# Kernel optimization log

Measured on AMD Instinct MI355X. Metric: run time of the kernel, lower is better.

The kernel has to match this reference:

```python
import jax, jax.numpy as jnp
import numpy as np
from jax import lax

SEQ_LEN, PRED_LEN, D_MODEL, ENC_IN, D_FF, N_LAYERS, N_HEADS = 336, 192, 512, 64, 2048, 2, 8
NUM_STEPS, COF, MARK, B, LABEL_LEN = 2, 0.1, 4, 32, 48


def _pos_emb(T, D):
    pos = np.arange(T)[:, None].astype(np.float32)
    div = np.exp(np.arange(0, D, 2).astype(np.float32) * (-np.log(10000.0) / D))
    pe = np.zeros((T, D), np.float32)
    pe[:, 0::2] = np.sin(pos * div)
    pe[:, 1::2] = np.cos(pos * div)
    return jnp.asarray(pe)


def _layer_norm(x, g, b):
    mu = x.mean(-1, keepdims=True)
    var = ((x - mu) ** 2).mean(-1, keepdims=True)
    return (x - mu) * lax.rsqrt(var + 1e-5) * g + b


def _embed(x, mark, conv_w, tf_w):
    # TokenEmbedding: circular Conv1d(kernel=3, pad=1) over time, no bias
    T = x.shape[1]
    xp = jnp.concatenate([x[:, -1:], x, x[:, :1]], axis=1)  # circular pad
    tok = sum(jnp.einsum('btc,cd->btd', xp[:, k:k + T], conv_w[k]) for k in range(3))
    return tok + _pos_emb(T, conv_w.shape[2])[None] + mark @ tf_w


def _block(x, p):
    Wq, Wk, Wv, Wo, bq, bk, bv, bo, g1, be1, W1, b1, W2, b2, g2, be2 = p
    Bb, T, D = x.shape
    dh = D // N_HEADS
    q = (x @ Wq + bq).reshape(Bb, T, N_HEADS, dh)
    k = (x @ Wk + bk).reshape(Bb, T, N_HEADS, dh)
    v = (x @ Wv + bv).reshape(Bb, T, N_HEADS, dh)
    att = jax.nn.softmax(jnp.einsum('bthd,bshd->bhts', q, k) / jnp.sqrt(jnp.float32(dh)), axis=-1)
    o = jnp.einsum('bhts,bshd->bthd', att, v).reshape(Bb, T, D) @ Wo + bo
    x = _layer_norm(x + o, g1, be1)
    ff = jax.nn.relu(x @ W1 + b1) @ W2 + b2
    return _layer_norm(x + ff, g2, be2)


def _gru(x, h, wih, whh, bih, bhh):
    gi = x @ wih.T + bih
    gh = h @ whh.T + bhh
    ir, iz, inn = jnp.split(gi, 3, axis=-1)
    hr, hz, hn = jnp.split(gh, 3, axis=-1)
    r = jax.nn.sigmoid(ir + hr)
    z = jax.nn.sigmoid(iz + hz)
    n = jnp.tanh(inn + r * hn)
    return (1.0 - z) * n + z * h


def _langevin(corrupt, cond, hx0, gru_p, score_w, alpha):
    # per-step GRU + energy-gradient update (Langevin refinement)
    def step(hx, xc):
        xi, ci = xc  # [B,C] each
        def energy(ri):
            h = _gru(jnp.concatenate([ri, ci], -1), hx, *gru_p)
            return (h @ score_w).sum() * COF, h
        g, h_new = jax.grad(energy, has_aux=True)(xi)
        return h_new, xi - alpha * g
    _, out = lax.scan(step, hx0, (corrupt.transpose(1, 0, 2), cond.transpose(1, 0, 2)))
    return out.transpose(1, 0, 2)  # [B,P,C]


def _forward(x_enc, x_mark_enc, batch_y, batch_y_mark, hx_init, token_conv_w, timefeat_w,
             Wq, Wk, Wv, Wo, bq, bk, bv, bo, ln1_g, ln1_b, W1, b1, W2, b2, ln2_g, ln2_b,
             pl1_w, pl1_b, pl2_w, pl2_b, proj_w, proj_b,
             gru_wih, gru_whh, gru_bih, gru_bhh, score_w, alpha):
    means = lax.stop_gradient(x_enc.mean(1, keepdims=True))
    xe = x_enc - means
    stdev = jnp.sqrt(xe.var(1, keepdims=True) + 1e-5)  # not detached in torch code
    xe = xe / stdev
    # predict_linear1 over time axis: [B,T,C] -> [B,P,C]
    pre = jnp.einsum('btc,pt->bpc', xe, pl1_w) + pl1_b[None, :, None]
    ymark = batch_y_mark[:, -PRED_LEN:, :]
    gru_p = (gru_wih, gru_whh, gru_bih, gru_bhh)
    local_loss = jnp.float32(0.0)
    out_dn = None
    for s in range(NUM_STEPS):
        corrupt = lax.stop_gradient(pre)
        corrupt = jnp.einsum('bpc,qp->bqc', corrupt, pl2_w) + pl2_b[None, :, None]
        emb = _embed(corrupt, ymark, token_conv_w, timefeat_w)
        for l in range(N_LAYERS):
            emb = _block(emb, (Wq[l], Wk[l], Wv[l], Wo[l], bq[l], bk[l], bv[l], bo[l],
                               ln1_g[l], ln1_b[l], W1[l], b1[l], W2[l], b2[l], ln2_g[l], ln2_b[l]))
        cond = emb @ proj_w.T + proj_b
        out = _langevin(corrupt, cond, hx_init[s], gru_p, score_w, alpha)
        pre = out
        out_dn = out * stdev[:, 0, :][:, None, :] + means[:, 0, :][:, None, :]
        local_loss = local_loss + jnp.mean(jnp.abs(out_dn - batch_y[:, -PRED_LEN:, :]))
    return out_dn, local_loss


def setup_inputs() -> dict:
    key = jax.random.key(0)
    ks = iter(jax.random.split(key, 64))
    r = lambda shape, s=0.02: jax.random.normal(next(ks), shape, dtype=jnp.float32) * s
    inp = dict(
        x_enc=jax.random.normal(next(ks), (B, SEQ_LEN, ENC_IN), dtype=jnp.float32),
        x_mark_enc=jax.random.normal(next(ks), (B, SEQ_LEN, MARK), dtype=jnp.float32),
        batch_y=jax.random.normal(next(ks), (B, LABEL_LEN + PRED_LEN, ENC_IN), dtype=jnp.float32),
        batch_y_mark=jax.random.normal(next(ks), (B, LABEL_LEN + PRED_LEN, MARK), dtype=jnp.float32),
        hx_init=jax.random.normal(next(ks), (NUM_STEPS, B, D_MODEL), dtype=jnp.float32),
        token_conv_w=r((3, ENC_IN, D_MODEL)),
        timefeat_w=r((MARK, D_MODEL)),
        Wq=r((N_LAYERS, D_MODEL, D_MODEL)), Wk=r((N_LAYERS, D_MODEL, D_MODEL)),
        Wv=r((N_LAYERS, D_MODEL, D_MODEL)), Wo=r((N_LAYERS, D_MODEL, D_MODEL)),
        bq=jnp.zeros((N_LAYERS, D_MODEL)), bk=jnp.zeros((N_LAYERS, D_MODEL)),
        bv=jnp.zeros((N_LAYERS, D_MODEL)), bo=jnp.zeros((N_LAYERS, D_MODEL)),
        ln1_g=jnp.ones((N_LAYERS, D_MODEL)), ln1_b=jnp.zeros((N_LAYERS, D_MODEL)),
        W1=r((N_LAYERS, D_MODEL, D_FF)), b1=jnp.zeros((N_LAYERS, D_FF)),
        W2=r((N_LAYERS, D_FF, D_MODEL)), b2=jnp.zeros((N_LAYERS, D_MODEL)),
        ln2_g=jnp.ones((N_LAYERS, D_MODEL)), ln2_b=jnp.zeros((N_LAYERS, D_MODEL)),
        pl1_w=r((PRED_LEN, SEQ_LEN), 0.05), pl1_b=jnp.zeros((PRED_LEN,)),
        pl2_w=r((PRED_LEN, PRED_LEN), 0.05), pl2_b=jnp.zeros((PRED_LEN,)),
        proj_w=r((ENC_IN, D_MODEL)), proj_b=jnp.zeros((ENC_IN,)),
        gru_wih=r((3 * D_MODEL, 2 * ENC_IN), 0.04), gru_whh=r((3 * D_MODEL, D_MODEL), 0.04),
        gru_bih=jnp.zeros((3 * D_MODEL,)), gru_bhh=jnp.zeros((3 * D_MODEL,)),
        score_w=r((D_MODEL,), 0.04),
        alpha=jnp.array([0.1], dtype=jnp.float32),
    )
    return inp


def reference(x_enc, x_mark_enc, batch_y, batch_y_mark, hx_init, token_conv_w, timefeat_w,
              Wq, Wk, Wv, Wo, bq, bk, bv, bo, ln1_g, ln1_b, W1, b1, W2, b2, ln2_g, ln2_b,
              pl1_w, pl1_b, pl2_w, pl2_b, proj_w, proj_b,
              gru_wih, gru_whh, gru_bih, gru_bhh, score_w, alpha):
    out, loss = _forward(x_enc, x_mark_enc, batch_y, batch_y_mark, hx_init, token_conv_w, timefeat_w,
                         Wq, Wk, Wv, Wo, bq, bk, bv, bo, ln1_g, ln1_b, W1, b1, W2, b2, ln2_g, ln2_b,
                         pl1_w, pl1_b, pl2_w, pl2_b, proj_w, proj_b,
                         gru_wih, gru_whh, gru_bih, gru_bhh, score_w, alpha)
    return out[:, -PRED_LEN:, :], loss
```

## Files before the change

kernel.cpp:

```cpp
#include <hip/hip_runtime.h>
#include <math.h>

#define BATCH 32
#define TT    192
#define DM    512
#define CIN   64
#define SEQL  336
#define DFF   2048
#define NH    8
#define COF   0.1f
#define OUTN  (BATCH*TT*CIN)

typedef _Float16 h2_t __attribute__((ext_vector_type(2)));
union H2U { unsigned int u; h2_t h; };

typedef short bf16x8 __attribute__((ext_vector_type(8)));
typedef float f32x4 __attribute__((ext_vector_type(4)));
typedef unsigned int u32x4 __attribute__((ext_vector_type(4)));

__device__ __forceinline__ unsigned short f2bf(float v) {
  union { float f; unsigned int u; } a; a.f = v;
  unsigned int r = (a.u + 0x7fffu + ((a.u >> 16) & 1u)) >> 16;
  return (unsigned short)r;
}

__device__ __forceinline__ int sd4(unsigned int a, unsigned int b, int c) {
#if __has_builtin(__builtin_amdgcn_sdot4)
  return __builtin_amdgcn_sdot4((int)a, (int)b, c, false);
#else
  c += (int)(signed char)(a & 0xff) * (int)(signed char)(b & 0xff);
  c += (int)(signed char)((a >> 8) & 0xff) * (int)(signed char)((b >> 8) & 0xff);
  c += (int)(signed char)((a >> 16) & 0xff) * (int)(signed char)((b >> 16) & 0xff);
  c += (int)(signed char)(a >> 24) * (int)(signed char)(b >> 24);
  return c;
#endif
}

__device__ __forceinline__ int sd16(u32x4 w, u32x4 h, int acc) {
  acc = sd4(w[0], h[0], acc); acc = sd4(w[1], h[1], acc);
  acc = sd4(w[2], h[2], acc); acc = sd4(w[3], h[3], acc);
  return acc;
}

__device__ __forceinline__ unsigned int packq4(const float* hp) {
  int a = (int)rintf(hp[0] * 15.875f); a = a < -127 ? -127 : (a > 127 ? 127 : a);
  int b = (int)rintf(hp[1] * 15.875f); b = b < -127 ? -127 : (b > 127 ? 127 : b);
  int c = (int)rintf(hp[2] * 15.875f); c = c < -127 ? -127 : (c > 127 ? 127 : c);
  int d = (int)rintf(hp[3] * 15.875f); d = d < -127 ? -127 : (d > 127 ? 127 : d);
  return (unsigned int)((a & 0xff) | ((b & 0xff) << 8) | ((c & 0xff) << 16) |
                        ((d & 0xff) << 24));
}


__global__ void zero_loss_kernel(float* loss) {
  if (threadIdx.x == 0) loss[0] = 0.f;
}

__global__ void zero_hqg_kernel(unsigned long long* p) {
  p[blockIdx.x * 256 + threadIdx.x] = 0ull;
}

__global__ void finalize_kernel(float* dout, const float* loss) {
  dout[OUTN] = loss[0] * (1.f / (float)OUTN);
}

__global__ void stats_kernel(const float* __restrict__ x, float* __restrict__ means,
                             float* __restrict__ stdev) {
  int b = blockIdx.x, c = threadIdx.x;
  const float* xb = x + (size_t)b * SEQL * CIN + c;
  float s = 0.f;
  for (int t = 0; t < SEQL; t++) s += xb[t * CIN];
  float mu = s * (1.f / SEQL);
  float s2 = 0.f;
  for (int t = 0; t < SEQL; t++) { float d = xb[t * CIN] - mu; s2 += d * d; }
  means[b * CIN + c] = mu;
  stdev[b * CIN + c] = sqrtf(s2 * (1.f / SEQL) + 1e-5f);
}

__global__ void pl1_kernel(const float* __restrict__ x, const float* __restrict__ means,
                           const float* __restrict__ stdev, const float* __restrict__ w,
                           const float* __restrict__ bias, float* __restrict__ pre) {
  int p = blockIdx.x, b = blockIdx.y, c = threadIdx.x;
  float mu = means[b * CIN + c];
  float inv = 1.f / stdev[b * CIN + c];
  const float* xb = x + (size_t)b * SEQL * CIN + c;
  const float* wp = w + p * SEQL;
  float acc = 0.f;
  for (int t = 0; t < SEQL; t++) acc += (xb[t * CIN] - mu) * wp[t];
  pre[((size_t)b * TT + p) * CIN + c] = acc * inv + bias[p];
}

__global__ void pl2_kernel(const float* __restrict__ pre, const float* __restrict__ w,
                           const float* __restrict__ bias, float* __restrict__ out) {
  int q = blockIdx.x, b = blockIdx.y, c = threadIdx.x;
  const float* pb = pre + (size_t)b * TT * CIN + c;
  const float* wq = w + q * TT;
  float acc = 0.f;
  for (int p = 0; p < TT; p++) acc += pb[p * CIN] * wq[p];
  out[((size_t)b * TT + q) * CIN + c] = acc + bias[q];
}

__global__ void embed_kernel(const float* __restrict__ corrupt, const float* __restrict__ ymark,
                             const float* __restrict__ conv_w, const float* __restrict__ tf_w,
                             float* __restrict__ emb, unsigned short* __restrict__ embB) {
  int t = blockIdx.x, b = blockIdx.y, d = threadIdx.x;
  __shared__ float xm[CIN], x0[CIN], xp[CIN], mk[4];
  int tm = (t + TT - 1) % TT, tp = (t + 1) % TT;
  if (d < CIN) {
    xm[d] = corrupt[((size_t)b * TT + tm) * CIN + d];
    x0[d] = corrupt[((size_t)b * TT + t) * CIN + d];
    xp[d] = corrupt[((size_t)b * TT + tp) * CIN + d];
  }
  if (d < 4) mk[d] = ymark[((size_t)b * 240 + 48 + t) * 4 + d];
  __syncthreads();
  float acc = 0.f;
  const float* w0 = conv_w + d;
  const float* w1 = conv_w + CIN * DM + d;
  const float* w2 = conv_w + 2 * CIN * DM + d;
  #pragma unroll 8
  for (int c = 0; c < CIN; c++)
    acc += xm[c] * w0[c * DM] + x0[c] * w1[c * DM] + xp[c] * w2[c * DM];
  int i2 = (d >> 1) * 2;
  float freq = expf((float)i2 * (-9.210340371976184f / (float)DM));
  float ang = (float)t * freq;
  float pe = (d & 1) ? cosf(ang) : sinf(ang);
  float mkacc = mk[0] * tf_w[d] + mk[1] * tf_w[DM + d] + mk[2] * tf_w[2 * DM + d] +
                mk[3] * tf_w[3 * DM + d];
  float val = acc + pe + mkacc;
  size_t o = ((size_t)b * TT + t) * DM + d;
  emb[o] = val;
  embB[o] = f2bf(val);
}

template <int TB, int RELU>
__global__ __launch_bounds__(256) void gemm_kernel(const float* __restrict__ A,
                                                   const float* __restrict__ B,
                                                   const float* __restrict__ bias,
                                                   float* __restrict__ C, int M, int N, int K) {
  __shared__ float As[16][68];
  __shared__ float Bs[16][68];
  int tid = threadIdx.x;
  int bn = blockIdx.x * 64, bm = blockIdx.y * 64;
  int tx = tid & 15, ty = tid >> 4;
  int row0 = ty * 4, col0 = tx * 4;
  float acc[4][4] = {};
  for (int k0 = 0; k0 < K; k0 += 16) {
    {
      int m = tid >> 2, kq = (tid & 3) << 2;
      float4 av = *(const float4*)&A[(size_t)(bm + m) * K + k0 + kq];
      As[kq + 0][m] = av.x; As[kq + 1][m] = av.y; As[kq + 2][m] = av.z; As[kq + 3][m] = av.w;
    }
    if (TB) {
      int n = tid >> 2, kq = (tid & 3) << 2;
      float4 bv = *(const float4*)&B[(size_t)(bn + n) * K + k0 + kq];
      Bs[kq + 0][n] = bv.x; Bs[kq + 1][n] = bv.y; Bs[kq + 2][n] = bv.z; Bs[kq + 3][n] = bv.w;
    } else {
      int kk = tid >> 4, nq = (tid & 15) << 2;
      float4 bv = *(const float4*)&B[(size_t)(k0 + kk) * N + bn + nq];
      *(float4*)&Bs[kk][nq] = bv;
    }
    __syncthreads();
    #pragma unroll
    for (int k = 0; k < 16; k++) {
      float4 a4 = *(const float4*)&As[k][row0];
      float4 b4 = *(const float4*)&Bs[k][col0];
      float a[4] = {a4.x, a4.y, a4.z, a4.w};
      float bb[4] = {b4.x, b4.y, b4.z, b4.w};
      #pragma unroll
      for (int i = 0; i < 4; i++)
        #pragma unroll
        for (int j = 0; j < 4; j++) acc[i][j] += a[i] * bb[j];
    }
    __syncthreads();
  }
  float bv[4] = {0.f, 0.f, 0.f, 0.f};
  if (bias) *(float4*)bv = *(const float4*)&bias[bn + col0];
  #pragma unroll
  for (int i = 0; i < 4; i++) {
    float ov[4];
    #pragma unroll
    for (int j = 0; j < 4; j++) {
      float v = acc[i][j] + bv[j];
      if (RELU) v = fmaxf(v, 0.f);
      ov[j] = v;
    }
    *(float4*)&C[(size_t)(bm + row0 + i) * N + bn + col0] = *(float4*)ov;
  }
}

template <int RELU, int WF32, int WBF16, int AXPY>
__global__ __launch_bounds__(256) void gemm_bf16_kernel(
    const unsigned short* __restrict__ A, const unsigned short* __restrict__ Bt,
    const float* __restrict__ bias, float* __restrict__ C, unsigned short* __restrict__ Cb,
    const float* __restrict__ R, const float* __restrict__ alphaPtr, int M, int N, int K) {
  __shared__ __align__(16) unsigned short As[128 * 40];
  __shared__ __align__(16) unsigned short Bs[128 * 40];
  int tid = threadIdx.x;
  int bm = blockIdx.y * 128, bn = blockIdx.x * 128;
  int wave = tid >> 6, lane = tid & 63;
  int wm = (wave >> 1) * 64, wn = (wave & 1) * 64;
  int r15 = lane & 15, q = lane >> 4;
  f32x4 acc[4][4] = {};
  int sr = tid >> 1, sh = (tid & 1) * 16;
  for (int k0 = 0; k0 < K; k0 += 32) {
    {
      const unsigned short* ap = &A[(size_t)(bm + sr) * K + k0 + sh];
      *(uint4*)&As[sr * 40 + sh] = *(const uint4*)ap;
      *(uint4*)&As[sr * 40 + sh + 8] = *(const uint4*)(ap + 8);
    }
    {
      const unsigned short* bp = &Bt[(size_t)(bn + sr) * K + k0 + sh];
      *(uint4*)&Bs[sr * 40 + sh] = *(const uint4*)bp;
      *(uint4*)&Bs[sr * 40 + sh + 8] = *(const uint4*)(bp + 8);
    }
    __syncthreads();
    bf16x8 af[4], bfr[4];
    #pragma unroll
    for (int mi = 0; mi < 4; mi++)
      af[mi] = *(const bf16x8*)&As[(wm + mi * 16 + r15) * 40 + q * 8];
    #pragma unroll
    for (int ni = 0; ni < 4; ni++)
      bfr[ni] = *(const bf16x8*)&Bs[(wn + ni * 16 + r15) * 40 + q * 8];
    #pragma unroll
    for (int mi = 0; mi < 4; mi++)
      #pragma unroll
      for (int ni = 0; ni < 4; ni++)
        acc[mi][ni] =
            __builtin_amdgcn_mfma_f32_16x16x32_bf16(af[mi], bfr[ni], acc[mi][ni], 0, 0, 0);
    __syncthreads();
  }
  float al = AXPY ? alphaPtr[0] : 0.f;
  #pragma unroll
  for (int mi = 0; mi < 4; mi++) {
    #pragma unroll
    for (int ni = 0; ni < 4; ni++) {
      int col = bn + wn + ni * 16 + r15;
      float bv = (bias && !AXPY) ? bias[col] : 0.f;
      #pragma unroll
      for (int v = 0; v < 4; v++) {
        int row = bm + wm + mi * 16 + q * 4 + v;
        float val = acc[mi][ni][v] + bv;
        if (RELU) val = fmaxf(val, 0.f);
        if (WF32) C[(size_t)row * N + col] = val;
        if (WBF16) Cb[(size_t)row * N + col] = f2bf(val);
        if (AXPY) {
          if (col < 64)
            C[(size_t)row * 64 + col] = R[(size_t)row * 64 + col] - al * val;
        }
      }
    }
  }
}

__global__ __launch_bounds__(256) void pack_transpose_bf16_kernel(
    const float* __restrict__ src, unsigned short* __restrict__ dst, int K, int N) {
  __shared__ unsigned short tile[64][65];
  int kb = blockIdx.x * 64, nb = blockIdx.y * 64;
  int tid = threadIdx.x;
  int tn = tid & 63, tk = tid >> 6;
  #pragma unroll
  for (int i = 0; i < 16; i++) {
    int k = tk + i * 4;
    tile[k][tn] = f2bf(src[(size_t)(kb + k) * N + nb + tn]);
  }
  __syncthreads();
  int tk2 = tid & 63, tn2 = tid >> 6;
  #pragma unroll
  for (int i = 0; i < 16; i++) {
    int n = tn2 + i * 4;
    dst[(size_t)(nb + n) * K + kb + tk2] = tile[tk2][n];
  }
}

__global__ void pack_bf16_kernel(const float* __restrict__ src, unsigned short* __restrict__ dst,
                                 int n) {
  int idx = blockIdx.x * 256 + threadIdx.x;
  if (idx < n) dst[idx] = f2bf(src[idx]);
}

__global__ void pack_wxproj_kernel(const float* __restrict__ wih,
                                   unsigned short* __restrict__ dst) {
  int idx = blockIdx.x * 256 + threadIdx.x;
  int k = idx % 1536, n = idx / 1536;
  float v = (n < 64) ? wih[(size_t)k * 128 + n] : 0.f;
  dst[idx] = f2bf(v);
}

__global__ void concat_qkv_bias_kernel(const float* __restrict__ bq, const float* __restrict__ bk,
                                       const float* __restrict__ bv, float* __restrict__ dst) {
  int l = blockIdx.y;
  int i = blockIdx.x * 256 + threadIdx.x;
  float v = (i < 512) ? bq[l * 512 + i]
                      : ((i < 1024) ? bk[l * 512 + i - 512] : bv[l * 512 + i - 1024]);
  dst[l * 1536 + i] = v;
}

__global__ __launch_bounds__(256) void attention_mfma_kernel(
    const unsigned short* __restrict__ qkv, unsigned short* __restrict__ attnO) {
  __shared__ __align__(16) unsigned short Ks[192 * 72];
  __shared__ __align__(16) unsigned short Vt[64 * 200];
  __shared__ __align__(16) float Ps[4][16 * 36];
  int h = blockIdx.x, b = blockIdx.y;
  int tid = threadIdx.x, wave = tid >> 6, lane = tid & 63;
  int m = lane & 15, q = lane >> 4;
  const unsigned short* Qg = qkv + (size_t)b * TT * 1536 + h * 64;
  const unsigned short* Kg = Qg + 512;
  const unsigned short* Vg = Qg + 1024;
  for (int idx = tid; idx < 192 * 8; idx += 256) {
    int s = idx >> 3, ch = (idx & 7) * 8;
    *(uint4*)&Ks[s * 72 + ch] = *(const uint4*)&Kg[(size_t)s * 1536 + ch];
  }
  for (int idx = tid; idx < 96 * 8; idx += 256) {
    int sp = idx >> 3, co = (idx & 7) * 8;
    uint4 v0 = *(const uint4*)&Vg[(size_t)(2 * sp) * 1536 + co];
    uint4 v1 = *(const uint4*)&Vg[(size_t)(2 * sp + 1) * 1536 + co];
    const unsigned short* e0 = (const unsigned short*)&v0;
    const unsigned short* e1 = (const unsigned short*)&v1;
    unsigned int* vtw = (unsigned int*)Vt;
    #pragma unroll
    for (int u = 0; u < 8; u++)
      vtw[(co + u) * 100 + sp] = (unsigned int)e0[u] | ((unsigned int)e1[u] << 16);
  }
  __syncthreads();
  float* ps = Ps[wave];
  for (int tile = wave; tile < 12; tile += 4) {
    int t0 = tile * 16;
    bf16x8 qf0 = *(const bf16x8*)&Qg[(size_t)(t0 + m) * 1536 + q * 8];
    bf16x8 qf1 = *(const bf16x8*)&Qg[(size_t)(t0 + m) * 1536 + 32 + q * 8];
    f32x4 S[12];
    #pragma unroll
    for (int nt = 0; nt < 12; nt++) {
      bf16x8 kf0 = *(const bf16x8*)&Ks[(nt * 16 + m) * 72 + q * 8];
      bf16x8 kf1 = *(const bf16x8*)&Ks[(nt * 16 + m) * 72 + 32 + q * 8];
      f32x4 a = {0.f, 0.f, 0.f, 0.f};
      a = __builtin_amdgcn_mfma_f32_16x16x32_bf16(qf0, kf0, a, 0, 0, 0);
      a = __builtin_amdgcn_mfma_f32_16x16x32_bf16(qf1, kf1, a, 0, 0, 0);
      S[nt] = a;
    }
    float mx[4] = {-1e30f, -1e30f, -1e30f, -1e30f};
    #pragma unroll
    for (int nt = 0; nt < 12; nt++)
      #pragma unroll
      for (int v = 0; v < 4; v++) {
        S[nt][v] *= 0.125f;
        mx[v] = fmaxf(mx[v], S[nt][v]);
      }
    #pragma unroll
    for (int d = 1; d < 16; d <<= 1) {
      #pragma unroll
      for (int v = 0; v < 4; v++) mx[v] = fmaxf(mx[v], __shfl_xor(mx[v], d));
    }
    float sm[4] = {0.f, 0.f, 0.f, 0.f};
    #pragma unroll
    for (int nt = 0; nt < 12; nt++)
      #pragma unroll
      for (int v = 0; v < 4; v++) {
        float e = __expf(S[nt][v] - mx[v]);
        S[nt][v] = e;
        sm[v] += e;
      }
    #pragma unroll
    for (int d = 1; d < 16; d <<= 1) {
      #pragma unroll
      for (int v = 0; v < 4; v++) sm[v] += __shfl_xor(sm[v], d);
    }
    float inv[4];
    #pragma unroll
    for (int v = 0; v < 4; v++) inv[v] = 1.f / sm[v];
    f32x4 o[4] = {};
    for (int kc = 0; kc < 6; kc++) {
      asm volatile("s_waitcnt lgkmcnt(0)" ::: "memory");
      #pragma unroll
      for (int half = 0; half < 2; half++) {
        int nt = 2 * kc + half;
        #pragma unroll
        for (int v = 0; v < 4; v++) ps[(q * 4 + v) * 36 + half * 16 + m] = S[nt][v];
      }
      asm volatile("s_waitcnt lgkmcnt(0)" ::: "memory");
      float4 p0 = *(const float4*)&ps[m * 36 + q * 8];
      float4 p1 = *(const float4*)&ps[m * 36 + q * 8 + 4];
      unsigned short tmp[8];
      tmp[0] = f2bf(p0.x); tmp[1] = f2bf(p0.y); tmp[2] = f2bf(p0.z); tmp[3] = f2bf(p0.w);
      tmp[4] = f2bf(p1.x); tmp[5] = f2bf(p1.y); tmp[6] = f2bf(p1.z); tmp[7] = f2bf(p1.w);
      bf16x8 pf = *(bf16x8*)tmp;
      #pragma unroll
      for (int nt2 = 0; nt2 < 4; nt2++) {
        bf16x8 vf = *(const bf16x8*)&Vt[(nt2 * 16 + m) * 200 + kc * 32 + q * 8];
        o[nt2] = __builtin_amdgcn_mfma_f32_16x16x32_bf16(pf, vf, o[nt2], 0, 0, 0);
      }
    }
    #pragma unroll
    for (int nt2 = 0; nt2 < 4; nt2++)
      #pragma unroll
      for (int v = 0; v < 4; v++) {
        size_t row = (size_t)b * TT + t0 + q * 4 + v;
        attnO[row * 512 + h * 64 + nt2 * 16 + m] = f2bf(o[nt2][v] * inv[v]);
      }
  }
}

__global__ __launch_bounds__(256) void ln_residual_kernel(float* __restrict__ x,
                                                          const float* __restrict__ res,
                                                          const float* __restrict__ g,
                                                          const float* __restrict__ b,
                                                          unsigned short* __restrict__ xb) {
  int row = blockIdx.x, tid = threadIdx.x;
  __shared__ float red[256];
  float* xr = x + (size_t)row * DM;
  const float* rr = res + (size_t)row * DM;
  float v0 = xr[tid] + rr[tid];
  float v1 = xr[tid + 256] + rr[tid + 256];
  red[tid] = v0 + v1;
  __syncthreads();
  for (int s = 128; s > 0; s >>= 1) {
    if (tid < s) red[tid] += red[tid + s];
    __syncthreads();
  }
  float mu = red[0] * (1.f / DM);
  __syncthreads();
  float d0 = v0 - mu, d1 = v1 - mu;
  red[tid] = d0 * d0 + d1 * d1;
  __syncthreads();
  for (int s = 128; s > 0; s >>= 1) {
    if (tid < s) red[tid] += red[tid + s];
    __syncthreads();
  }
  float rstd = rsqrtf(red[0] * (1.f / DM) + 1e-5f);
  float o0 = d0 * rstd * g[tid] + b[tid];
  float o1 = d1 * rstd * g[tid + 256] + b[tid + 256];
  xr[tid] = o0;
  xr[tid + 256] = o1;
  xb[(size_t)row * DM + tid] = f2bf(o0);
  xb[(size_t)row * DM + tid + 256] = f2bf(o1);
}

__global__ void xcat_kernel(const float* __restrict__ corrupt, const float* __restrict__ cond,
                            unsigned short* __restrict__ xcatB) {
  int r = blockIdx.x, tid = threadIdx.x;
  float v = (tid < 64) ? corrupt[(size_t)r * 64 + tid] : cond[(size_t)r * 64 + (tid - 64)];
  xcatB[(size_t)r * 128 + tid] = f2bf(v);
}

__global__ void pack_whh_q8_kernel(const float* __restrict__ whh, signed char* __restrict__ whhJ,
                                   float* __restrict__ sws) {
  int row = blockIdx.x;
  int lane = threadIdx.x;
  const float* src = whh + (size_t)row * 512;
  float mx = 0.f;
  for (int k = lane; k < 512; k += 64) mx = fmaxf(mx, fabsf(src[k]));
  for (int off = 32; off > 0; off >>= 1) mx = fmaxf(mx, __shfl_xor(mx, off));
  float inv = (mx > 0.f) ? 127.f / mx : 0.f;
  if (lane == 0) sws[row] = (mx / 127.f) * (8.f / 127.f);
  int g = row >> 9, jj = row & 511;
  int quad = jj >> 7, jl = jj & 127;
  for (int k = lane; k < 512; k += 64) {
    int qv = (int)rintf(src[k] * inv);
    qv = qv < -127 ? -127 : (qv > 127 ? 127 : qv);
    int kh = k >> 6, u = (k >> 4) & 3, m = k & 15;
    whhJ[((size_t)(((quad * 128 + jl) * 8 + kh) * 4 + u) * 3 + g) * 16 + m] = (signed char)qv;
  }
}

__global__ __launch_bounds__(1024, 4) void langevin_scan_kernel(
    const float* __restrict__ gi_all, const float* __restrict__ hx0,
    const signed char* __restrict__ whhJ, const float* __restrict__ sws,
    const float* __restrict__ bhh, const float* __restrict__ score_w,
    unsigned short* __restrict__ dgiB, unsigned long long* __restrict__ hqg, int tagBase) {
  int b = blockIdx.x, quad = blockIdx.y;
  int tid = threadIdx.x;
  __shared__ __align__(16) unsigned int hqp[2][160];
  int jl = tid >> 3, kh = tid & 7;
  int j = quad * 128 + jl;
  bool act = (kh == 0);
  float bhr = 0.f, bhz = 0.f, bhn = 0.f, sw = 0.f, swr = 0.f, swz = 0.f, swn = 0.f, h = 0.f;
  if (act) {
    bhr = bhh[j]; bhz = bhh[512 + j]; bhn = bhh[1024 + j];
    sw = score_w[j] * COF;
    swr = sws[j]; swz = sws[512 + j]; swn = sws[1024 + j];
    h = hx0[(size_t)b * 512 + j];
  }
  if (tid < 128) {
    float4 hv = *(const float4*)&hx0[(size_t)b * 512 + tid * 4];
    float tmp[4] = {hv.x, hv.y, hv.z, hv.w};
    hqp[0][(tid >> 4) * 20 + (tid & 15)] = packq4(tmp);
  }
  const u32x4* wbase = (const u32x4*)whhJ + (size_t)((quad * 128 + jl) * 8 + kh) * 12;
  u32x4 wreg[12];
  #pragma unroll
  for (int i = 0; i < 12; i++) wreg[i] = wbase[i];
  #pragma unroll
  for (int i = 0; i < 12; i++) asm volatile("" : "+v"(wreg[i]));
  float gir = 0.f, giz = 0.f, gin = 0.f, gir1 = 0.f, giz1 = 0.f, gin1 = 0.f;
  if (act) {
    const float* g0 = &gi_all[(size_t)b * TT * 1536];
    gir = g0[j]; giz = g0[512 + j]; gin = g0[1024 + j];
    const float* g1 = g0 + 1536;
    gir1 = g1[j]; giz1 = g1[512 + j]; gin1 = g1[1024 + j];
  }
  __syncthreads();
  for (int t = 0; t < TT; t++) {
    int rb = t & 1;
    int ir = 0, iz = 0, in_ = 0;
    #pragma unroll
    for (int u = 0; u < 4; u++) {
      u32x4 hqv = *(const u32x4*)&hqp[rb][kh * 20 + u * 4];
      ir = sd16(wreg[u * 3 + 0], hqv, ir);
      iz = sd16(wreg[u * 3 + 1], hqv, iz);
      in_ = sd16(wreg[u * 3 + 2], hqv, in_);
    }
    #pragma unroll
    for (int d = 1; d < 8; d <<= 1) {
      ir += __shfl_xor(ir, d);
      iz += __shfl_xor(iz, d);
      in_ += __shfl_xor(in_, d);
    }
    int qv = 0;
    float r = 0.f, z = 0.f, n = 0.f, hnv = 0.f, hj = 0.f;
    if (act) {
      float gr = (float)ir * swr, gz = (float)iz * swz, gn2 = (float)in_ * swn;
      r = 1.f / (1.f + expf(-(gir + gr + bhr)));
      z = 1.f / (1.f + expf(-(giz + gz + bhz)));
      hnv = gn2 + bhn;
      n = tanhf(gin + r * hnv);
      hj = h;
      h = (1.f - z) * n + z * hj;
      int q = (int)rintf(h * 15.875f);
      qv = q < -127 ? -127 : (q > 127 ? 127 : q);
    }
    int l = tid & 63;
    int q1 = __shfl(qv, (l + 8) & 63);
    int q2 = __shfl(qv, (l + 16) & 63);
    int q3 = __shfl(qv, (l + 24) & 63);
    bool ex = (t + 1 < TT);
    int wb = (t + 1) & 1;
    unsigned tag = (unsigned)(tagBase + t + 1);
    if (ex && (tid & 31) == 0) {
      unsigned word = (unsigned)(qv & 0xff) | ((unsigned)(q1 & 0xff) << 8) |
                      ((unsigned)(q2 & 0xff) << 16) | ((unsigned)(q3 & 0xff) << 24);
      int w = quad * 32 + (tid >> 5);
      hqp[wb][(w >> 4) * 20 + (w & 15)] = word;
      __hip_atomic_store(&hqg[((size_t)wb * BATCH + b) * 128 + w],
                         ((unsigned long long)tag << 32) | (unsigned long long)word,
                         __ATOMIC_RELAXED, __HIP_MEMORY_SCOPE_AGENT);
    }
    float dg0 = 0.f, dg1 = 0.f, dg2 = 0.f;
    if (act) {
      float dinn = sw * (1.f - z) * (1.f - n * n);
      dg0 = dinn * hnv * r * (1.f - r);
      dg1 = sw * (hj - n) * z * (1.f - z);
      dg2 = dinn;
    }
    if (ex && kh == 1 && jl < 96) {
      int o = jl >> 5;
      int oq = (quad + 1 + o) & 3;
      int w = oq * 32 + (jl & 31);
      unsigned long long* p = &hqg[((size_t)wb * BATCH + b) * 128 + w];
      unsigned long long v = __hip_atomic_load(p, __ATOMIC_RELAXED, __HIP_MEMORY_SCOPE_AGENT);
      while ((unsigned)(v >> 32) != tag) {
        __builtin_amdgcn_s_sleep(1);
        v = __hip_atomic_load(p, __ATOMIC_RELAXED, __HIP_MEMORY_SCOPE_AGENT);
      }
      hqp[wb][(w >> 4) * 20 + (w & 15)] = (unsigned)v;
    }
    __builtin_amdgcn_sched_barrier(0);
    float girP = 0.f, gizP = 0.f, ginP = 0.f;
    if (act && t + 2 < TT) {
      const float* gp = &gi_all[((size_t)b * TT + t + 2) * 1536];
      girP = gp[j]; gizP = gp[512 + j]; ginP = gp[1024 + j];
    }
    if (act) {
      size_t drow = ((size_t)b * TT + t) * 1536;
      dgiB[drow + j] = f2bf(dg0);
      dgiB[drow + 512 + j] = f2bf(dg1);
      dgiB[drow + 1024 + j] = f2bf(dg2);
    }
    if (ex) __syncthreads();
    gir = gir1; giz = giz1; gin = gin1;
    gir1 = girP; giz1 = gizP; gin1 = ginP;
  }
}

__global__ __launch_bounds__(256) void denorm_loss_kernel(
    const float* __restrict__ outb, const float* __restrict__ stdev,
    const float* __restrict__ means, const float* __restrict__ y, float* __restrict__ dout,
    float* __restrict__ loss) {
  int idx = blockIdx.x * 256 + threadIdx.x;
  int tid = threadIdx.x;
  int c = idx & 63;
  int bt = idx >> 6;
  int t = bt % TT, b = bt / TT;
  float od = outb[idx] * stdev[b * CIN + c] + means[b * CIN + c];
  dout[idx] = od;
  float diff = fabsf(od - y[((size_t)b * 240 + 48 + t) * CIN + c]);
  __shared__ float red[256];
  red[tid] = diff;
  __syncthreads();
  for (int s = 128; s > 0; s >>= 1) {
    if (tid < s) red[tid] += red[tid + s];
    __syncthreads();
  }
  if (tid == 0) atomicAdd(loss, red[0]);
}

extern "C" void kernel_launch(void* const* d_in, const int* in_sizes, int n_in, void* d_out,
                              int out_size, void* d_ws, size_t ws_size, hipStream_t stream) {
  const float* x_enc = (const float*)d_in[0];
  const float* batch_y = (const float*)d_in[2];
  const float* y_mark = (const float*)d_in[3];
  const float* hx_init = (const float*)d_in[4];
  const float* conv_w = (const float*)d_in[5];
  const float* tf_w = (const float*)d_in[6];
  const float* Wq = (const float*)d_in[7];
  const float* Wk = (const float*)d_in[8];
  const float* Wv = (const float*)d_in[9];
  const float* Wo = (const float*)d_in[10];
  const float* bq = (const float*)d_in[11];
  const float* bk = (const float*)d_in[12];
  const float* bv = (const float*)d_in[13];
  const float* bo = (const float*)d_in[14];
  const float* ln1_g = (const float*)d_in[15];
  const float* ln1_b = (const float*)d_in[16];
  const float* W1 = (const float*)d_in[17];
  const float* b1 = (const float*)d_in[18];
  const float* W2 = (const float*)d_in[19];
  const float* b2 = (const float*)d_in[20];
  const float* ln2_g = (const float*)d_in[21];
  const float* ln2_b = (const float*)d_in[22];
  const float* pl1_w = (const float*)d_in[23];
  const float* pl1_b = (const float*)d_in[24];
  const float* pl2_w = (const float*)d_in[25];
  const float* pl2_b = (const float*)d_in[26];
  const float* proj_w = (const float*)d_in[27];
  const float* proj_b = (const float*)d_in[28];
  const float* gru_wih = (const float*)d_in[29];
  const float* gru_whh = (const float*)d_in[30];
  const float* gru_bih = (const float*)d_in[31];
  const float* gru_bhh = (const float*)d_in[32];
  const float* score_w = (const float*)d_in[33];
  const float* alpha = (const float*)d_in[34];
  float* dout = (float*)d_out;

  float* W = (float*)d_ws;
  size_t off = 0;
  float* means = W + off;   off += 2048;
  float* stdev = W + off;   off += 2048;
  float* lossacc = W + off; off += 64;
  float* preA = W + off;    off += (size_t)OUTN;
  float* outA = W + off;    off += (size_t)OUTN;
  float* outB = W + off;    off += (size_t)OUTN;
  float* corrupt = W + off; off += (size_t)OUTN;
  float* cond = W + off;    off += (size_t)OUTN;
  signed char* whhJ = (signed char*)(W + off); off += 786432 / 4;
  float* sws = W + off;     off += 1536;
  unsigned long long* hqg = (unsigned long long*)(W + off); off += 2 * BATCH * 128 * 2;
  float* emb = W + off;     off += (size_t)BATCH * TT * DM;
  float* Kb = W + off;      off += (size_t)BATCH * TT * DM;
  float* gi_all = W + off;  off += (size_t)BATCH * TT * 1536;
  unsigned short* embB = (unsigned short*)(W + off);  off += (size_t)BATCH * TT * DM / 2;
  unsigned short* qkvB = (unsigned short*)(W + off);  off += (size_t)BATCH * TT * 1536 / 2;
  unsigned short* attnOB = (unsigned short*)(W + off); off += (size_t)BATCH * TT * DM / 2;
  unsigned short* FFbB = (unsigned short*)(W + off);  off += (size_t)BATCH * TT * DFF / 2;
  unsigned short* xcatB = (unsigned short*)(W + off); off += (size_t)BATCH * TT * 128 / 2;
  float* bqkv = W + off;    off += 2 * 1536;
  unsigned short* WxProjB = (unsigned short*)(W + off); off += (size_t)128 * 1536 / 2;
  unsigned short* wT = (unsigned short*)(W + off);
  const size_t SQ = (size_t)DM * DM;
  const size_t SFF = (size_t)DM * DFF;
  const size_t LAYER = 4 * SQ + 2 * SFF;
  unsigned short* wihB = wT + 2 * LAYER;
  off += (2 * LAYER + (size_t)1536 * 128) / 2 + 64;
  unsigned short* dgiB = qkvB;

  const int M = BATCH * TT;

  zero_loss_kernel<<<1, 64, 0, stream>>>(lossacc);
  zero_hqg_kernel<<<32, 256, 0, stream>>>(hqg);
  stats_kernel<<<BATCH, 64, 0, stream>>>(x_enc, means, stdev);
  pl1_kernel<<<dim3(TT, BATCH), 64, 0, stream>>>(x_enc, means, stdev, pl1_w, pl1_b, preA);
  pack_whh_q8_kernel<<<1536, 64, 0, stream>>>(gru_whh, whhJ, sws);
  pack_wxproj_kernel<<<(128 * 1536) / 256, 256, 0, stream>>>(gru_wih, WxProjB);
  concat_qkv_bias_kernel<<<dim3(6, 2), 256, 0, stream>>>(bq, bk, bv, bqkv);
  for (int l = 0; l < 2; l++) {
    unsigned short* base = wT + (size_t)l * LAYER;
    pack_transpose_bf16_kernel<<<dim3(8, 8), 256, 0, stream>>>(Wq + (size_t)l * SQ, base, DM, DM);
    pack_transpose_bf16_kernel<<<dim3(8, 8), 256, 0, stream>>>(Wk + (size_t)l * SQ, base + SQ, DM, DM);
    pack_transpose_bf16_kernel<<<dim3(8, 8), 256, 0, stream>>>(Wv + (size_t)l * SQ, base + 2 * SQ, DM, DM);
    pack_transpose_bf16_kernel<<<dim3(8, 8), 256, 0, stream>>>(Wo + (size_t)l * SQ, base + 3 * SQ, DM, DM);
    pack_transpose_bf16_kernel<<<dim3(8, 32), 256, 0, stream>>>(W1 + (size_t)l * SFF, base + 4 * SQ, DM, DFF);
    pack_transpose_bf16_kernel<<<dim3(32, 8), 256, 0, stream>>>(W2 + (size_t)l * SFF, base + 4 * SQ + SFF, DFF, DM);
  }
  pack_bf16_kernel<<<(1536 * 128) / 256, 256, 0, stream>>>(gru_wih, wihB, 1536 * 128);

  const float* pre = preA;
  float* outs[2] = {outA, outB};
  for (int s = 0; s < 2; s++) {
    pl2_kernel<<<dim3(TT, BATCH), 64, 0, stream>>>(pre, pl2_w, pl2_b, corrupt);
    embed_kernel<<<dim3(TT, BATCH), DM, 0, stream>>>(corrupt, y_mark, conv_w, tf_w, emb, embB);
    for (int l = 0; l < 2; l++) {
      unsigned short* base = wT + (size_t)l * LAYER;
      gemm_bf16_kernel<0, 0, 1, 0><<<dim3(1536 / 128, M / 128), 256, 0, stream>>>(
          embB, base, bqkv + l * 1536, nullptr, qkvB, nullptr, nullptr, M, 1536, DM);
      attention_mfma_kernel<<<dim3(NH, BATCH), 256, 0, stream>>>(qkvB, attnOB);
      gemm_bf16_kernel<0, 1, 0, 0><<<dim3(DM / 128, M / 128), 256, 0, stream>>>(
          attnOB, base + 3 * SQ, bo + l * DM, Kb, nullptr, nullptr, nullptr, M, DM, DM);
      ln_residual_kernel<<<M, 256, 0, stream>>>(emb, Kb, ln1_g + l * DM, ln1_b + l * DM, embB);
      gemm_bf16_kernel<1, 0, 1, 0><<<dim3(DFF / 128, M / 128), 256, 0, stream>>>(
          embB, base + 4 * SQ, b1 + l * DFF, nullptr, FFbB, nullptr, nullptr, M, DFF, DM);
      gemm_bf16_kernel<0, 1, 0, 0><<<dim3(DM / 128, M / 128), 256, 0, stream>>>(
          FFbB, base + 4 * SQ + SFF, b2 + l * DM, Kb, nullptr, nullptr, nullptr, M, DM, DFF);
      ln_residual_kernel<<<M, 256, 0, stream>>>(emb, Kb, ln2_g + l * DM, ln2_b + l * DM, embB);
    }
    gemm_kernel<1, 0><<<dim3(CIN / 64, M / 64), 256, 0, stream>>>(
        emb, proj_w, proj_b, cond, M, CIN, DM);
    xcat_kernel<<<M, 128, 0, stream>>>(corrupt, cond, xcatB);
    gemm_bf16_kernel<0, 1, 0, 0><<<dim3(1536 / 128, M / 128), 256, 0, stream>>>(
        xcatB, wihB, gru_bih, gi_all, nullptr, nullptr, nullptr, M, 1536, 128);
    langevin_scan_kernel<<<dim3(BATCH, 4), 1024, 0, stream>>>(
        gi_all, hx_init + (size_t)s * BATCH * DM, whhJ, sws, gru_bhh, score_w, dgiB, hqg,
        s * TT);
    gemm_bf16_kernel<0, 0, 0, 1><<<dim3(1, M / 128), 256, 0, stream>>>(
        dgiB, WxProjB, nullptr, outs[s], nullptr, corrupt, alpha, M, 128, 1536);
    denorm_loss_kernel<<<OUTN / 256, 256, 0, stream>>>(outs[s], stdev, means, batch_y, dout,
                                                       lossacc);
    pre = outs[s];
  }
  finalize_kernel<<<1, 1, 0, stream>>>(dout, lossacc);
}
```

Measured before the change: 2.435 ms.

## Run each batch's GRU scan in one workgroup, streaming weights from cache

The Langevin GRU scan moves from four cooperating workgroups per batch element, which exchanged hidden-state chunks through tagged global atomics and spin-waits, to a single 1024-thread workgroup per batch element that keeps the whole quantized hidden state in shared memory. Each thread now covers half the K dimension of one hidden unit. Because the int8 recurrent weights are no longer resident in registers, they are re-read from global memory/L2 every step, and the weight packing layout is changed so these reads coalesce. This removes the cross-workgroup polling latency and the hqg zeroing kernel. The cost is fewer workgroups (32 instead of 128) and about 768KB of weight traffic per step per block, served from cache.

Measured after the change: 3.751 ms. 54.1% more time.

```diff
diff --git a/kernel.cpp b/kernel.cpp
--- a/kernel.cpp
+++ b/kernel.cpp
@@ -54,10 +54,6 @@
 
 __global__ void zero_loss_kernel(float* loss) {
   if (threadIdx.x == 0) loss[0] = 0.f;
-}
-
-__global__ void zero_hqg_kernel(unsigned long long* p) {
-  p[blockIdx.x * 256 + threadIdx.x] = 0ull;
 }
 
 __global__ void finalize_kernel(float* dout, const float* loss) {
@@ -441,7 +437,7 @@
   xcatB[(size_t)r * 128 + tid] = f2bf(v);
 }
 
-__global__ void pack_whh_q8_kernel(const float* __restrict__ whh, signed char* __restrict__ whhJ,
+__global__ void pack_whh_q8_kernel(const float* __restrict__ whh, signed char* __restrict__ whhS,
                                    float* __restrict__ sws) {
   int row = blockIdx.x;
   int lane = threadIdx.x;
@@ -451,69 +447,65 @@
   for (int off = 32; off > 0; off >>= 1) mx = fmaxf(mx, __shfl_xor(mx, off));
   float inv = (mx > 0.f) ? 127.f / mx : 0.f;
   if (lane == 0) sws[row] = (mx / 127.f) * (8.f / 127.f);
-  int g = row >> 9, jj = row & 511;
-  int quad = jj >> 7, jl = jj & 127;
+  int g = row >> 9, j = row & 511;
   for (int k = lane; k < 512; k += 64) {
     int qv = (int)rintf(src[k] * inv);
     qv = qv < -127 ? -127 : (qv > 127 ? 127 : qv);
-    int kh = k >> 6, u = (k >> 4) & 3, m = k & 15;
-    whhJ[((size_t)(((quad * 128 + jl) * 8 + kh) * 4 + u) * 3 + g) * 16 + m] = (signed char)qv;
+    int kh = k >> 8, u = (k >> 4) & 15, m = k & 15;
+    whhS[((size_t)(u * 3 + g) * 1024 + j * 2 + kh) * 16 + m] = (signed char)qv;
   }
 }
 
 __global__ __launch_bounds__(1024, 4) void langevin_scan_kernel(
     const float* __restrict__ gi_all, const float* __restrict__ hx0,
-    const signed char* __restrict__ whhJ, const float* __restrict__ sws,
+    const signed char* __restrict__ whhS, const float* __restrict__ sws,
     const float* __restrict__ bhh, const float* __restrict__ score_w,
-    unsigned short* __restrict__ dgiB, unsigned long long* __restrict__ hqg, int tagBase) {
-  int b = blockIdx.x, quad = blockIdx.y;
+    unsigned short* __restrict__ dgiB) {
+  int b = blockIdx.x;
   int tid = threadIdx.x;
-  __shared__ __align__(16) unsigned int hqp[2][160];
-  int jl = tid >> 3, kh = tid & 7;
-  int j = quad * 128 + jl;
+  __shared__ __align__(16) unsigned char hqb[2][512];
+  int jl = tid >> 1, kh = tid & 1;
   bool act = (kh == 0);
   float bhr = 0.f, bhz = 0.f, bhn = 0.f, sw = 0.f, swr = 0.f, swz = 0.f, swn = 0.f, h = 0.f;
   if (act) {
-    bhr = bhh[j]; bhz = bhh[512 + j]; bhn = bhh[1024 + j];
-    sw = score_w[j] * COF;
-    swr = sws[j]; swz = sws[512 + j]; swn = sws[1024 + j];
-    h = hx0[(size_t)b * 512 + j];
+    bhr = bhh[jl]; bhz = bhh[512 + jl]; bhn = bhh[1024 + jl];
+    sw = score_w[jl] * COF;
+    swr = sws[jl]; swz = sws[512 + jl]; swn = sws[1024 + jl];
+    h = hx0[(size_t)b * 512 + jl];
   }
   if (tid < 128) {
     float4 hv = *(const float4*)&hx0[(size_t)b * 512 + tid * 4];
     float tmp[4] = {hv.x, hv.y, hv.z, hv.w};
-    hqp[0][(tid >> 4) * 20 + (tid & 15)] = packq4(tmp);
-  }
-  const u32x4* wbase = (const u32x4*)whhJ + (size_t)((quad * 128 + jl) * 8 + kh) * 12;
-  u32x4 wreg[12];
-  #pragma unroll
-  for (int i = 0; i < 12; i++) wreg[i] = wbase[i];
-  #pragma unroll
-  for (int i = 0; i < 12; i++) asm volatile("" : "+v"(wreg[i]));
+    ((unsigned int*)hqb[0])[tid] = packq4(tmp);
+  }
   float gir = 0.f, giz = 0.f, gin = 0.f, gir1 = 0.f, giz1 = 0.f, gin1 = 0.f;
   if (act) {
     const float* g0 = &gi_all[(size_t)b * TT * 1536];
-    gir = g0[j]; giz = g0[512 + j]; gin = g0[1024 + j];
+    gir = g0[jl]; giz = g0[512 + jl]; gin = g0[1024 + jl];
     const float* g1 = g0 + 1536;
-    gir1 = g1[j]; giz1 = g1[512 + j]; gin1 = g1[1024 + j];
-  }
+    gir1 = g1[jl]; giz1 = g1[512 + jl]; gin1 = g1[1024 + jl];
+  }
+  size_t toff = (size_t)tid * 16;
   __syncthreads();
   for (int t = 0; t < TT; t++) {
-    int rb = t & 1;
+    int rb = t & 1, wb = rb ^ 1;
+    const unsigned char* hr = &hqb[rb][kh * 256];
+    const char* p = (const char*)whhS;
     int ir = 0, iz = 0, in_ = 0;
-    #pragma unroll
-    for (int u = 0; u < 4; u++) {
-      u32x4 hqv = *(const u32x4*)&hqp[rb][kh * 20 + u * 4];
-      ir = sd16(wreg[u * 3 + 0], hqv, ir);
-      iz = sd16(wreg[u * 3 + 1], hqv, iz);
-      in_ = sd16(wreg[u * 3 + 2], hqv, in_);
-    }
-    #pragma unroll
-    for (int d = 1; d < 8; d <<= 1) {
-      ir += __shfl_xor(ir, d);
-      iz += __shfl_xor(iz, d);
-      in_ += __shfl_xor(in_, d);
-    }
+    #pragma unroll 4
+    for (int u = 0; u < 16; u++) {
+      u32x4 hc = *(const u32x4*)(hr + u * 16);
+      u32x4 wr_ = *(const u32x4*)(p + toff);
+      u32x4 wz_ = *(const u32x4*)(p + 16384 + toff);
+      u32x4 wn_ = *(const u32x4*)(p + 32768 + toff);
+      p += 49152;
+      ir = sd16(wr_, hc, ir);
+      iz = sd16(wz_, hc, iz);
+      in_ = sd16(wn_, hc, in_);
+    }
+    ir += __shfl_xor(ir, 1);
+    iz += __shfl_xor(iz, 1);
+    in_ += __shfl_xor(in_, 1);
     int qv = 0;
     float r = 0.f, z = 0.f, n = 0.f, hnv = 0.f, hj = 0.f;
     if (act) {
@@ -526,55 +518,21 @@
       h = (1.f - z) * n + z * hj;
       int q = (int)rintf(h * 15.875f);
       qv = q < -127 ? -127 : (q > 127 ? 127 : q);
-    }
-    int l = tid & 63;
-    int q1 = __shfl(qv, (l + 8) & 63);
-    int q2 = __shfl(qv, (l + 16) & 63);
-    int q3 = __shfl(qv, (l + 24) & 63);
-    bool ex = (t + 1 < TT);
-    int wb = (t + 1) & 1;
-    unsigned tag = (unsigned)(tagBase + t + 1);
-    if (ex && (tid & 31) == 0) {
-      unsigned word = (unsigned)(qv & 0xff) | ((unsigned)(q1 & 0xff) << 8) |
-                      ((unsigned)(q2 & 0xff) << 16) | ((unsigned)(q3 & 0xff) << 24);
-      int w = quad * 32 + (tid >> 5);
-      hqp[wb][(w >> 4) * 20 + (w & 15)] = word;
-      __hip_atomic_store(&hqg[((size_t)wb * BATCH + b) * 128 + w],
-                         ((unsigned long long)tag << 32) | (unsigned long long)word,
-                         __ATOMIC_RELAXED, __HIP_MEMORY_SCOPE_AGENT);
-    }
-    float dg0 = 0.f, dg1 = 0.f, dg2 = 0.f;
+      hqb[wb][jl] = (unsigned char)qv;
+    }
     if (act) {
       float dinn = sw * (1.f - z) * (1.f - n * n);
-      dg0 = dinn * hnv * r * (1.f - r);
-      dg1 = sw * (hj - n) * z * (1.f - z);
-      dg2 = dinn;
-    }
-    if (ex && kh == 1 && jl < 96) {
-      int o = jl >> 5;
-      int oq = (quad + 1 + o) & 3;
-      int w = oq * 32 + (jl & 31);
-      unsigned long long* p = &hqg[((size_t)wb * BATCH + b) * 128 + w];
-      unsigned long long v = __hip_atomic_load(p, __ATOMIC_RELAXED, __HIP_MEMORY_SCOPE_AGENT);
-      while ((unsigned)(v >> 32) != tag) {
-        __builtin_amdgcn_s_sleep(1);
-        v = __hip_atomic_load(p, __ATOMIC_RELAXED, __HIP_MEMORY_SCOPE_AGENT);
-      }
-      hqp[wb][(w >> 4) * 20 + (w & 15)] = (unsigned)v;
-    }
-    __builtin_amdgcn_sched_barrier(0);
+      size_t drow = ((size_t)b * TT + t) * 1536;
+      dgiB[drow + jl] = f2bf(dinn * hnv * r * (1.f - r));
+      dgiB[drow + 512 + jl] = f2bf(sw * (hj - n) * z * (1.f - z));
+      dgiB[drow + 1024 + jl] = f2bf(dinn);
+    }
     float girP = 0.f, gizP = 0.f, ginP = 0.f;
     if (act && t + 2 < TT) {
       const float* gp = &gi_all[((size_t)b * TT + t + 2) * 1536];
-      girP = gp[j]; gizP = gp[512 + j]; ginP = gp[1024 + j];
-    }
-    if (act) {
-      size_t drow = ((size_t)b * TT + t) * 1536;
-      dgiB[drow + j] = f2bf(dg0);
-      dgiB[drow + 512 + j] = f2bf(dg1);
-      dgiB[drow + 1024 + j] = f2bf(dg2);
-    }
-    if (ex) __syncthreads();
+      girP = gp[jl]; gizP = gp[512 + jl]; ginP = gp[1024 + jl];
+    }
+    if (t + 1 < TT) __syncthreads();
     gir = gir1; giz = giz1; gin = gin1;
     gir1 = girP; giz1 = gizP; gin1 = ginP;
   }
@@ -652,7 +610,6 @@
   float* cond = W + off;    off += (size_t)OUTN;
   signed char* whhJ = (signed char*)(W + off); off += 786432 / 4;
   float* sws = W + off;     off += 1536;
-  unsigned long long* hqg = (unsigned long long*)(W + off); off += 2 * BATCH * 128 * 2;
   float* emb = W + off;     off += (size_t)BATCH * TT * DM;
   float* Kb = W + off;      off += (size_t)BATCH * TT * DM;
   float* gi_all = W + off;  off += (size_t)BATCH * TT * 1536;
@@ -674,7 +631,6 @@
   const int M = BATCH * TT;
 
   zero_loss_kernel<<<1, 64, 0, stream>>>(lossacc);
-  zero_hqg_kernel<<<32, 256, 0, stream>>>(hqg);
   stats_kernel<<<BATCH, 64, 0, stream>>>(x_enc, means, stdev);
   pl1_kernel<<<dim3(TT, BATCH), 64, 0, stream>>>(x_enc, means, stdev, pl1_w, pl1_b, preA);
   pack_whh_q8_kernel<<<1536, 64, 0, stream>>>(gru_whh, whhJ, sws);
@@ -715,9 +671,8 @@
     xcat_kernel<<<M, 128, 0, stream>>>(corrupt, cond, xcatB);
     gemm_bf16_kernel<0, 1, 0, 0><<<dim3(1536 / 128, M / 128), 256, 0, stream>>>(
         xcatB, wihB, gru_bih, gi_all, nullptr, nullptr, nullptr, M, 1536, 128);
-    langevin_scan_kernel<<<dim3(BATCH, 4), 1024, 0, stream>>>(
-        gi_all, hx_init + (size_t)s * BATCH * DM, whhJ, sws, gru_bhh, score_w, dgiB, hqg,
-        s * TT);
+    langevin_scan_kernel<<<dim3(BATCH), 1024, 0, stream>>>(
+        gi_all, hx_init + (size_t)s * BATCH * DM, whhJ, sws, gru_bhh, score_w, dgiB);
     gemm_bf16_kernel<0, 0, 0, 1><<<dim3(1, M / 128), 256, 0, stream>>>(
         dgiB, WxProjB, nullptr, outs[s], nullptr, corrupt, alpha, M, 128, 1536);
     denorm_loss_kernel<<<OUTN / 256, 256, 0, stream>>>(outs[s], stdev, means, batch_y, dout,
```
